# Optimization experiments

Hardware: AMD Instinct MI355X
Metric: run time of the kernel (lower is better)

The kernel has to match this reference:

```python
import jax, jax.numpy as jnp
import numpy as np

K = 1024          # num_embeddings
D = 64            # embedding_dim
TEMP = 1.0        # cfg.temperature
EPS = 1e-10


def setup_inputs() -> dict:
    key = jax.random.key(0)
    k1, k2 = jax.random.split(key)
    return {
        "inputs": jax.random.normal(k1, (16, 2048, D), dtype=jnp.float32),
        "embedding": jax.random.normal(k2, (K, D), dtype=jnp.float32),
        "code_count": jnp.ones((K,), dtype=jnp.float32),
    }


def _distances(flat, embedding):
    return ((flat ** 2).sum(axis=1, keepdims=True)
            + (embedding ** 2).sum(axis=1)
            - 2.0 * flat @ embedding.T)


def reference(inputs, embedding, code_count):
    B = inputs.shape[0]
    flat = inputs.reshape(-1, D)                      # [N, D]
    N = flat.shape[0]

    d = _distances(flat, embedding)                   # [N, K]
    idx = jnp.argmin(d, axis=1)                       # [N]

    # one-hot @ codebook == gather by index
    quantized = embedding[idx].reshape(inputs.shape)

    commitment_loss = jnp.mean((jax.lax.stop_gradient(quantized) - inputs) ** 2)

    # ortho loss over used codes (code_count >= 1), via masking (jit-safe)
    mask = (code_count >= 1.0).astype(inputs.dtype)   # [K]
    n_used = mask.sum()
    normed = embedding / jnp.clip(
        jnp.linalg.norm(embedding, axis=1, keepdims=True), 1e-12)
    normed = normed * mask[:, None]                   # zero out unused rows
    cos = normed @ normed.T                           # [K, K]
    ortho_loss = (cos ** 2).sum() / (n_used ** 2) - 1.0 / n_used

    # entropy loss over softmax(-d / T)
    prob = jax.nn.softmax(-d / TEMP, axis=1)          # [N, K]
    entropy_loss = -jnp.mean(jnp.sum(prob * jnp.log(prob + EPS), axis=1))
    entropy_loss = entropy_loss / jnp.log2(jnp.asarray(K, inputs.dtype))

    # straight-through estimator
    quantized_st = inputs + jax.lax.stop_gradient(quantized - inputs)

    # perplexity from code usage histogram (mean of one-hot encodings)
    avg_probs = jnp.zeros((K,), inputs.dtype).at[idx].add(1.0) / N
    perplexity = jnp.exp(-jnp.sum(avg_probs * jnp.log(avg_probs + EPS)))

    coverage = mask.sum() / K
    indices = idx.reshape(B, -1)

    return (quantized_st, commitment_loss, ortho_loss, entropy_loss,
            perplexity, coverage, indices)
```

## Files before the change

### kernel.cpp

```cpp
#include <hip/hip_runtime.h>
#include <math.h>

#define N_ROWS  32768
#define K_CODES 1024
#define D_DIM   64
#define NSPLIT  4
#define C_SHIFT 30.0f
#define LOG2E_F 1.4426950408889634f
#define LN2_F   0.6931471805599453f
#define TAU     0.25f

#define WS_CNT    0
#define WS_E2C    6144
#define PART_STRIDE (NSPLIT * N_ROWS)
#define WS_PART_S  8192
#define WS_PART_U  (8192 + PART_STRIDE)
#define WS_PART_M1 (8192 + 2 * PART_STRIDE)
#define WS_PART_M2 (8192 + 3 * PART_STRIDE)
#define CHUNK_F4  260
#define MAIN_CHUNKS 16
#define WS_EB      (8192 + 4 * PART_STRIDE)
#define WS_GP      (WS_EB + 64 * CHUNK_F4 * 4)
#define WS_HB      (WS_GP + 16 * 4096)
#define WS_PH      (WS_HB + 16 * K_CODES)
#define WS_PC      (WS_PH + 512)

#define OUT_Q      0
#define OUT_COMMIT 2097152
#define OUT_ORTHO  2097153
#define OUT_ENT    2097154
#define OUT_PERP   2097155
#define OUT_COV    2097156
#define OUT_IDX    2097157

typedef __attribute__((ext_vector_type(8))) _Float16 f16x8;
typedef __attribute__((ext_vector_type(4))) float f32x4;

__device__ inline unsigned umaxu(unsigned a, unsigned b) { return a > b ? a : b; }
__device__ inline unsigned uminu(unsigned a, unsigned b) { return a < b ? a : b; }

__device__ inline float keyval(unsigned u) {
    unsigned b = (u & 0x80000000u) ? (u ^ 0x80000000u) : ~u;
    return __uint_as_float(b);
}

__device__ inline void decomp2x8(const float* v, f16x8& h, f16x8& m) {
#pragma unroll
    for (int i = 0; i < 8; ++i) {
        _Float16 hh = (_Float16)v[i];
        h[i] = hh;
        m[i] = (_Float16)(v[i] - (float)hh);
    }
}

__global__ __launch_bounds__(256) void vq_prep_ortho(const float* __restrict__ emb,
                                                     const float* __restrict__ cc,
                                                     float* __restrict__ ws) {
    __shared__ float srows[64][64];
    __shared__ float rn2[64];
    const int t = threadIdx.x;

    if (blockIdx.x < 16) {
        if (blockIdx.x == 0 && t == 0) ((int*)ws)[WS_CNT] = 0;

        const int tid  = blockIdx.x * 256 + t;
        const int c    = tid >> 6;
        const int lane = tid & 63;
        const int col  = lane & 15;
        const int kg   = lane >> 4;
        const int code = c * 16 + col;
        float4* EB4 = (float4*)(ws + WS_EB);
#pragma unroll
        for (int s = 0; s < 2; ++s) {
            const float* ep = emb + (size_t)code * D_DIM + s * 32 + kg * 8;
            float4 A4 = *(const float4*)ep;
            float4 B4 = *(const float4*)(ep + 4);
            float v[8] = {A4.x, A4.y, A4.z, A4.w, B4.x, B4.y, B4.z, B4.w};
            union { f16x8 h; float4 f; } th, tm;
            decomp2x8(v, th.h, tm.h);
            const int base = c * CHUNK_F4;
            EB4[base + (s * 2 + 0) * 64 + lane] = th.f;
            EB4[base + (s * 2 + 1) * 64 + lane] = tm.f;
        }
        if (kg == 0) {
            const float4* e4 = (const float4*)(emb + (size_t)code * D_DIM);
            float ssum = 0.f;
#pragma unroll
            for (int j = 0; j < 16; ++j) {
                float4 v = e4[j];
                ssum += v.x * v.x + v.y * v.y + v.z * v.z + v.w * v.w;
            }
            float e2c = ssum + C_SHIFT;
            ws[WS_E2C + code] = e2c;
            ((float*)(EB4 + c * CHUNK_F4 + 256))[col] = e2c * LOG2E_F;
        }
        return;
    }

    const int ob = blockIdx.x - 16;
    const int k0 = ob * 64;
    const int rb = t >> 4;
    const int c4 = (t & 15) << 2;

#pragma unroll
    for (int i = 0; i < 4; ++i) {
        const int r = i * 16 + rb;
        float4 v = *(const float4*)(emb + (size_t)(k0 + r) * D_DIM + c4);
        *(float4*)(&srows[r][c4]) = v;
        float ss = v.x * v.x + v.y * v.y + v.z * v.z + v.w * v.w;
        ss += __shfl_down(ss, 8, 16);
        ss += __shfl_down(ss, 4, 16);
        ss += __shfl_down(ss, 2, 16);
        ss += __shfl_down(ss, 1, 16);
        if ((t & 15) == 0) {
            float nrm = fmaxf(sqrtf(ss), 1e-12f);
            float m = (cc[k0 + r] >= 1.0f) ? 1.0f : 0.0f;
            rn2[r] = m / (nrm * nrm);
        }
    }
    __syncthreads();

    const int a  = t >> 2;
    const int b0 = (t & 3) << 4;
    float acc[16];
#pragma unroll
    for (int i = 0; i < 16; ++i) acc[i] = 0.f;

#pragma unroll 4
    for (int k = 0; k < 64; ++k) {
        float na = srows[k][a] * rn2[k];
        const float* rbp = &srows[k][b0];
#pragma unroll
        for (int i = 0; i < 16; ++i) acc[i] = fmaf(na, rbp[i], acc[i]);
    }
#pragma unroll
    for (int i = 0; i < 16; ++i)
        ws[WS_GP + ob * 4096 + a * 64 + b0 + i] = acc[i];
}

#define MFMA_F16 __builtin_amdgcn_mfma_f32_16x16x32_f16

__global__ __launch_bounds__(256)
void vq_main(const float* __restrict__ inp, float* __restrict__ ws) {
    __shared__ float4 sbuf[3][256];
    const int t    = threadIdx.x;
    const int lane = t & 63;
    const int wave = t >> 6;
    const int col  = lane & 15;
    const int kg   = lane >> 4;
    const int rg   = blockIdx.x >> 2;
    const int sp   = blockIdx.x & 3;
    const int row  = rg * 64 + wave * 16 + col;

    f16x8 xh0, xm0, xh1, xm1;
    {
        const float* xp = inp + (size_t)row * D_DIM + kg * 8;
        float4 A4 = *(const float4*)xp;
        float4 B4 = *(const float4*)(xp + 4);
        float v[8] = {A4.x, A4.y, A4.z, A4.w, B4.x, B4.y, B4.z, B4.w};
        decomp2x8(v, xh0, xm0);
        A4 = *(const float4*)(xp + 32);
        B4 = *(const float4*)(xp + 36);
        float w[8] = {A4.x, A4.y, A4.z, A4.w, B4.x, B4.y, B4.z, B4.w};
        decomp2x8(w, xh1, xm1);
    }

    const float4* EBp = (const float4*)(ws + WS_EB)
                      + (size_t)sp * MAIN_CHUNKS * CHUNK_F4;

    float sa[4], ua[4];
    unsigned m1[4], m2[4];
#pragma unroll
    for (int q = 0; q < 4; ++q) {
        sa[q] = 0.f; ua[q] = 0.f;
        m1[q] = 0u; m2[q] = 0u;
    }

    sbuf[0][t] = EBp[t];
    sbuf[1][t] = EBp[CHUNK_F4 + t];

#pragma unroll 1
    for (int c = 0; c < MAIN_CHUNKS; ++c) {
        __syncthreads();
        float4 gn;
        if (c + 2 < MAIN_CHUNKS) gn = EBp[(size_t)(c + 2) * CHUNK_F4 + t];

        const f16x8* pb = (const f16x8*)&sbuf[c % 3][0];
        const float e2v = ((const float*)(EBp + (size_t)c * CHUNK_F4 + 256))[col];

        f32x4 acc = {0.f, 0.f, 0.f, 0.f};
        {
            f16x8 bh0 = pb[0 * 64 + lane];
            f16x8 bm0 = pb[1 * 64 + lane];
            acc = MFMA_F16(xh0, bh0, acc, 0, 0, 0);
            acc = MFMA_F16(xm0, bh0, acc, 0, 0, 0);
            acc = MFMA_F16(xh0, bm0, acc, 0, 0, 0);
            acc = MFMA_F16(xm0, bm0, acc, 0, 0, 0);
        }
        {
            f16x8 bh1 = pb[2 * 64 + lane];
            f16x8 bm1 = pb[3 * 64 + lane];
            acc = MFMA_F16(xh1, bh1, acc, 0, 0, 0);
            acc = MFMA_F16(xm1, bh1, acc, 0, 0, 0);
            acc = MFMA_F16(xh1, bm1, acc, 0, 0, 0);
            acc = MFMA_F16(xm1, bm1, acc, 0, 0, 0);
        }

        const unsigned embedv = 255u - (unsigned)(c * 16 + col);
#pragma unroll
        for (int q = 0; q < 4; ++q) {
            float g = fmaf(2.0f * LOG2E_F, acc[q], -e2v);
            float pw;
            asm("v_exp_f32 %0, %1" : "=v"(pw) : "v"(g));
            sa[q] += pw;
            ua[q] = fmaf(pw, g, ua[q]);
            int gb = __float_as_int(g);
            unsigned u = (unsigned)(gb ^ ((gb >> 31) | 0x80000000));
            unsigned key = (u & 0xFFFFFF00u) | embedv;
            m2[q] = uminu(umaxu(key, m2[q]), m1[q]);
            m1[q] = umaxu(m1[q], key);
        }

        if (c + 2 < MAIN_CHUNKS) sbuf[(c + 2) % 3][t] = gn;
    }

#pragma unroll
    for (int off = 1; off < 16; off <<= 1) {
#pragma unroll
        for (int q = 0; q < 4; ++q) {
            sa[q] += __shfl_xor(sa[q], off);
            ua[q] += __shfl_xor(ua[q], off);
            unsigned p1 = (unsigned)__shfl_xor((int)m1[q], off);
            unsigned p2 = (unsigned)__shfl_xor((int)m2[q], off);
            unsigned lo = uminu(m1[q], p1);
            m1[q] = umaxu(m1[q], p1);
            m2[q] = umaxu(lo, umaxu(m2[q], p2));
        }
    }

    if (col == 0) {
#pragma unroll
        for (int q = 0; q < 4; ++q) {
            const int r  = rg * 64 + wave * 16 + kg * 4 + q;
            const int pi = sp * N_ROWS + r;
            ws[WS_PART_S  + pi] = sa[q];
            ws[WS_PART_U  + pi] = ua[q];
            ws[WS_PART_M1 + pi] = __uint_as_float(m1[q]);
            ws[WS_PART_M2 + pi] = __uint_as_float(m2[q]);
        }
    }
}

__global__ __launch_bounds__(256) void vq_combine(const float* __restrict__ inp,
                                                  const float* __restrict__ emb,
                                                  float* __restrict__ ws,
                                                  float* __restrict__ out) {
    __shared__ float shH[4], shC[4];
    const int t    = threadIdx.x;
    const int lane = t & 63;
    const int wave = t >> 6;
    const int l    = t & 3;
    const int row  = blockIdx.x * 64 + (t >> 2);
    const int qb   = lane & ~3;

    const int pi = l * N_ROWS + row;
    float    Sl = ws[WS_PART_S  + pi];
    float    Ul = ws[WS_PART_U  + pi];
    unsigned K1 = __float_as_uint(ws[WS_PART_M1 + pi]);
    unsigned K2 = __float_as_uint(ws[WS_PART_M2 + pi]);
    float    G1 = keyval(K1);

    float S = 0.f, U2 = 0.f, Gmax = -1e30f;
#pragma unroll
    for (int k = 0; k < 4; ++k) {
        S  += __shfl(Sl, qb + k);
        U2 += __shfl(Ul, qb + k);
        Gmax = fmaxf(Gmax, __shfl(G1, qb + k));
    }

    float4 Xq[4];
    const float4* xr = (const float4*)(inp + (size_t)row * D_DIM);
#pragma unroll
    for (int k = 0; k < 4; ++k) Xq[k] = xr[l + 4 * k];

    float bestg = -1e30f; int I = K_CODES;
#pragma unroll 1
    for (int j = 0; j < 8; ++j) {
        const int sp = j >> 1;
        const unsigned kk = (unsigned)__shfl((int)((j & 1) ? K2 : K1), qb + sp);
        const float v = keyval(kk);
        if (v < Gmax - TAU) continue;
        const int c = sp * 256 + 255 - (int)(kk & 255u);
        const float4* e4 = (const float4*)(emb + (size_t)c * D_DIM);
        float d = 0.f;
#pragma unroll
        for (int k = 0; k < 4; ++k) {
            float4 ev = e4[l + 4 * k];
            float4 xv = Xq[k];
            d = fmaf(ev.x, xv.x, d); d = fmaf(ev.y, xv.y, d);
            d = fmaf(ev.z, xv.z, d); d = fmaf(ev.w, xv.w, d);
        }
        float dA = __shfl(d, qb + 0) + __shfl(d, qb + 1);
        float dB = __shfl(d, qb + 2) + __shfl(d, qb + 3);
        float g  = fmaf(2.0f, dA + dB, -ws[WS_E2C + c]);
        if (g > bestg || (g == bestg && c < I)) { bestg = g; I = c; }
    }

    float H = logf(S) - (U2 * LN2_F) / S;

    if (l == 0) out[OUT_IDX + row] = (float)I;

    const float4* q4 = (const float4*)(emb + (size_t)I * D_DIM);
    float4* oq = (float4*)out + (size_t)row * 16;
    float cs = 0.f;
#pragma unroll
    for (int k = 0; k < 4; ++k) {
        float4 q = q4[l + 4 * k], x = Xq[k];
        float dx = q.x - x.x, dy = q.y - x.y, dz = q.z - x.z, dw = q.w - x.w;
        cs += dx * dx + dy * dy + dz * dz + dw * dw;
        float4 o;
        o.x = x.x + dx; o.y = x.y + dy; o.z = x.z + dz; o.w = x.w + dw;
        oq[l + 4 * k] = o;
    }

    float Hc = (l == 0) ? H : 0.f;
#pragma unroll
    for (int off = 32; off; off >>= 1) {
        Hc += __shfl_down(Hc, off);
        cs += __shfl_down(cs, off);
    }
    if (lane == 0) { shH[wave] = Hc; shC[wave] = cs; }
    __syncthreads();
    if (t == 0) {
        ws[WS_PH + blockIdx.x] = shH[0] + shH[1] + shH[2] + shH[3];
        ws[WS_PC + blockIdx.x] = shC[0] + shC[1] + shC[2] + shC[3];
    }
}

__global__ __launch_bounds__(256) void vq_hist_fin(const float* __restrict__ cc,
                                                   float* __restrict__ ws,
                                                   float* __restrict__ out) {
    __shared__ int h[K_CODES];
    __shared__ int lastFlag;
    __shared__ float red[5][4];
    const int t = threadIdx.x;
#pragma unroll
    for (int i = 0; i < 4; ++i) h[t + 256 * i] = 0;
    __syncthreads();
    const int base = blockIdx.x * 2048;
#pragma unroll
    for (int i = 0; i < 8; ++i) {
        int idx = (int)out[OUT_IDX + base + t + 256 * i];
        atomicAdd(&h[idx], 1);
    }
    __syncthreads();
#pragma unroll
    for (int i = 0; i < 4; ++i) {
        const int k = t + 256 * i;
        ws[WS_HB + blockIdx.x * K_CODES + k] = (float)h[k];
    }
    __threadfence();
    __syncthreads();
    if (t == 0) {
        int old = __hip_atomic_fetch_add((int*)ws + WS_CNT, 1,
                                         __ATOMIC_ACQ_REL,
                                         __HIP_MEMORY_SCOPE_AGENT);
        lastFlag = (old == 15);
    }
    __syncthreads();
    if (!lastFlag) return;

    float hp = 0.f, gg = 0.f, nu = 0.f, hh = 0.f, cm = 0.f;
    for (int k = t; k < K_CODES; k += 256) {
        float s = 0.f;
#pragma unroll
        for (int b = 0; b < 16; ++b)
            s += __hip_atomic_load(ws + WS_HB + b * K_CODES + k,
                                   __ATOMIC_RELAXED, __HIP_MEMORY_SCOPE_AGENT);
        float p = s * (1.0f / (float)N_ROWS);
        hp += p * logf(p + 1e-10f);
        nu += (cc[k] >= 1.0f) ? 1.0f : 0.0f;
    }
    for (int i = t; i < 4096; i += 256) {
        float s = 0.f;
#pragma unroll
        for (int b = 0; b < 16; ++b) s += ws[WS_GP + b * 4096 + i];
        gg = fmaf(s, s, gg);
    }
    for (int i = t; i < 512; i += 256) {
        hh += ws[WS_PH + i];
        cm += ws[WS_PC + i];
    }
#pragma unroll
    for (int off = 32; off; off >>= 1) {
        hp += __shfl_down(hp, off);
        gg += __shfl_down(gg, off);
        nu += __shfl_down(nu, off);
        hh += __shfl_down(hh, off);
        cm += __shfl_down(cm, off);
    }
    if ((t & 63) == 0) {
        const int w = t >> 6;
        red[0][w] = hp; red[1][w] = gg; red[2][w] = nu;
        red[3][w] = hh; red[4][w] = cm;
    }
    __syncthreads();
    if (t == 0) {
        float hsum = red[0][0] + red[0][1] + red[0][2] + red[0][3];
        float gsum = red[1][0] + red[1][1] + red[1][2] + red[1][3];
        float nuv  = red[2][0] + red[2][1] + red[2][2] + red[2][3];
        float hacc = red[3][0] + red[3][1] + red[3][2] + red[3][3];
        float cacc = red[4][0] + red[4][1] + red[4][2] + red[4][3];
        out[OUT_PERP]   = expf(-hsum);
        out[OUT_ENT]    = hacc * (1.0f / (float)N_ROWS) * 0.1f;
        out[OUT_COMMIT] = cacc * (1.0f / ((float)N_ROWS * (float)D_DIM));
        out[OUT_ORTHO]  = gsum / (nuv * nuv) - 1.0f / nuv;
        out[OUT_COV]    = nuv * (1.0f / (float)K_CODES);
    }
}

extern "C" void kernel_launch(void* const* d_in, const int* in_sizes, int n_in,
                              void* d_out, int out_size, void* d_ws, size_t ws_size,
                              hipStream_t stream) {
    const float* inp = (const float*)d_in[0];
    const float* emb = (const float*)d_in[1];
    const float* cc  = (const float*)d_in[2];
    float* out = (float*)d_out;
    float* ws  = (float*)d_ws;

    vq_prep_ortho<<<32, 256, 0, stream>>>(emb, cc, ws);
    vq_main<<<(N_ROWS / 64) * NSPLIT, 256, 0, stream>>>(inp, ws);
    vq_combine<<<N_ROWS / 64, 256, 0, stream>>>(inp, emb, ws, out);
    vq_hist_fin<<<16, 256, 0, stream>>>(cc, ws, out);
}
```

Before: 119.8 us.

## Fuse combine stage into main kernel and drop codebook split across blocks

Each block now scans all 1024 codes itself instead of splitting the codebook four ways across blocks, keeping per-quarter top-2 keys and the softmax partial sums in shared memory. The argmin rescoring, quantized output and loss partials that used to live in a separate combine kernel now run in the tail of the main kernel. This removes one launch and the global round trip of partial results. In exchange, the grid shrinks from 2048 to 512 blocks, which reduces parallelism and latency hiding, and each block runs a longer serial chunk loop.

```diff
diff --git a/kernel.cpp b/kernel.cpp
--- a/kernel.cpp
+++ b/kernel.cpp
@@ -4,7 +4,6 @@
 #define N_ROWS  32768
 #define K_CODES 1024
 #define D_DIM   64
-#define NSPLIT  4
 #define C_SHIFT 30.0f
 #define LOG2E_F 1.4426950408889634f
 #define LN2_F   0.6931471805599453f
@@ -12,14 +11,9 @@
 
 #define WS_CNT    0
 #define WS_E2C    6144
-#define PART_STRIDE (NSPLIT * N_ROWS)
-#define WS_PART_S  8192
-#define WS_PART_U  (8192 + PART_STRIDE)
-#define WS_PART_M1 (8192 + 2 * PART_STRIDE)
-#define WS_PART_M2 (8192 + 3 * PART_STRIDE)
 #define CHUNK_F4  260
-#define MAIN_CHUNKS 16
-#define WS_EB      (8192 + 4 * PART_STRIDE)
+#define ALL_CHUNKS 64
+#define WS_EB      8192
 #define WS_GP      (WS_EB + 64 * CHUNK_F4 * 4)
 #define WS_HB      (WS_GP + 16 * 4096)
 #define WS_PH      (WS_HB + 16 * K_CODES)
@@ -141,15 +135,18 @@
 #define MFMA_F16 __builtin_amdgcn_mfma_f32_16x16x32_f16
 
 __global__ __launch_bounds__(256)
-void vq_main(const float* __restrict__ inp, float* __restrict__ ws) {
+void vq_main(const float* __restrict__ inp, const float* __restrict__ emb,
+             float* __restrict__ ws, float* __restrict__ out) {
     __shared__ float4 sbuf[3][256];
+    __shared__ unsigned cK[4][16][4][2];
+    __shared__ float sS[4][16], sU[4][16];
+    __shared__ float shH[4], shC[4];
     const int t    = threadIdx.x;
     const int lane = t & 63;
     const int wave = t >> 6;
     const int col  = lane & 15;
     const int kg   = lane >> 4;
-    const int rg   = blockIdx.x >> 2;
-    const int sp   = blockIdx.x & 3;
+    const int rg   = blockIdx.x;
     const int row  = rg * 64 + wave * 16 + col;
 
     f16x8 xh0, xm0, xh1, xm1;
@@ -165,8 +162,7 @@
         decomp2x8(w, xh1, xm1);
     }
 
-    const float4* EBp = (const float4*)(ws + WS_EB)
-                      + (size_t)sp * MAIN_CHUNKS * CHUNK_F4;
+    const float4* EBp = (const float4*)(ws + WS_EB);
 
     float sa[4], ua[4];
     unsigned m1[4], m2[4];
@@ -180,10 +176,10 @@
     sbuf[1][t] = EBp[CHUNK_F4 + t];
 
 #pragma unroll 1
-    for (int c = 0; c < MAIN_CHUNKS; ++c) {
+    for (int c = 0; c < ALL_CHUNKS; ++c) {
         __syncthreads();
         float4 gn;
-        if (c + 2 < MAIN_CHUNKS) gn = EBp[(size_t)(c + 2) * CHUNK_F4 + t];
+        if (c + 2 < ALL_CHUNKS) gn = EBp[(size_t)(c + 2) * CHUNK_F4 + t];
 
         const f16x8* pb = (const f16x8*)&sbuf[c % 3][0];
         const float e2v = ((const float*)(EBp + (size_t)c * CHUNK_F4 + 256))[col];
@@ -206,7 +202,7 @@
             acc = MFMA_F16(xm1, bm1, acc, 0, 0, 0);
         }
 
-        const unsigned embedv = 255u - (unsigned)(c * 16 + col);
+        const unsigned embedv = 255u - (unsigned)((c & 15) * 16 + col);
 #pragma unroll
         for (int q = 0; q < 4; ++q) {
             float g = fmaf(2.0f * LOG2E_F, acc[q], -e2v);
@@ -221,7 +217,31 @@
             m1[q] = umaxu(m1[q], key);
         }
 
-        if (c + 2 < MAIN_CHUNKS) sbuf[(c + 2) % 3][t] = gn;
+        if ((c & 15) == 15) {
+            const int qt = c >> 4;
+#pragma unroll
+            for (int off = 1; off < 16; off <<= 1) {
+#pragma unroll
+                for (int q = 0; q < 4; ++q) {
+                    unsigned p1 = (unsigned)__shfl_xor((int)m1[q], off);
+                    unsigned p2 = (unsigned)__shfl_xor((int)m2[q], off);
+                    unsigned lo = uminu(m1[q], p1);
+                    m1[q] = umaxu(m1[q], p1);
+                    m2[q] = umaxu(lo, umaxu(m2[q], p2));
+                }
+            }
+            if (col == 0) {
+#pragma unroll
+                for (int q = 0; q < 4; ++q) {
+                    cK[wave][kg * 4 + q][qt][0] = m1[q];
+                    cK[wave][kg * 4 + q][qt][1] = m2[q];
+                }
+            }
+#pragma unroll
+            for (int q = 0; q < 4; ++q) { m1[q] = 0u; m2[q] = 0u; }
+        }
+
+        if (c + 2 < ALL_CHUNKS) sbuf[(c + 2) % 3][t] = gn;
     }
 
 #pragma unroll
@@ -230,67 +250,43 @@
         for (int q = 0; q < 4; ++q) {
             sa[q] += __shfl_xor(sa[q], off);
             ua[q] += __shfl_xor(ua[q], off);
-            unsigned p1 = (unsigned)__shfl_xor((int)m1[q], off);
-            unsigned p2 = (unsigned)__shfl_xor((int)m2[q], off);
-            unsigned lo = uminu(m1[q], p1);
-            m1[q] = umaxu(m1[q], p1);
-            m2[q] = umaxu(lo, umaxu(m2[q], p2));
-        }
-    }
-
+        }
+    }
     if (col == 0) {
 #pragma unroll
         for (int q = 0; q < 4; ++q) {
-            const int r  = rg * 64 + wave * 16 + kg * 4 + q;
-            const int pi = sp * N_ROWS + r;
-            ws[WS_PART_S  + pi] = sa[q];
-            ws[WS_PART_U  + pi] = ua[q];
-            ws[WS_PART_M1 + pi] = __uint_as_float(m1[q]);
-            ws[WS_PART_M2 + pi] = __uint_as_float(m2[q]);
-        }
-    }
-}
-
-__global__ __launch_bounds__(256) void vq_combine(const float* __restrict__ inp,
-                                                  const float* __restrict__ emb,
-                                                  float* __restrict__ ws,
-                                                  float* __restrict__ out) {
-    __shared__ float shH[4], shC[4];
-    const int t    = threadIdx.x;
-    const int lane = t & 63;
-    const int wave = t >> 6;
+            sS[wave][kg * 4 + q] = sa[q];
+            sU[wave][kg * 4 + q] = ua[q];
+        }
+    }
+    __syncthreads();
+
     const int l    = t & 3;
-    const int row  = blockIdx.x * 64 + (t >> 2);
+    const int rloc = (t >> 2) & 15;
+    const int wsrc = t >> 6;
+    const int frow = rg * 64 + wsrc * 16 + rloc;
     const int qb   = lane & ~3;
 
-    const int pi = l * N_ROWS + row;
-    float    Sl = ws[WS_PART_S  + pi];
-    float    Ul = ws[WS_PART_U  + pi];
-    unsigned K1 = __float_as_uint(ws[WS_PART_M1 + pi]);
-    unsigned K2 = __float_as_uint(ws[WS_PART_M2 + pi]);
-    float    G1 = keyval(K1);
-
-    float S = 0.f, U2 = 0.f, Gmax = -1e30f;
-#pragma unroll
-    for (int k = 0; k < 4; ++k) {
-        S  += __shfl(Sl, qb + k);
-        U2 += __shfl(Ul, qb + k);
-        Gmax = fmaxf(Gmax, __shfl(G1, qb + k));
-    }
+    float S  = sS[wsrc][rloc];
+    float U2 = sU[wsrc][rloc];
+
+    float Gmax = -1e30f;
+#pragma unroll
+    for (int qt = 0; qt < 4; ++qt)
+        Gmax = fmaxf(Gmax, keyval(cK[wsrc][rloc][qt][0]));
 
     float4 Xq[4];
-    const float4* xr = (const float4*)(inp + (size_t)row * D_DIM);
+    const float4* xr = (const float4*)(inp + (size_t)frow * D_DIM);
 #pragma unroll
     for (int k = 0; k < 4; ++k) Xq[k] = xr[l + 4 * k];
 
     float bestg = -1e30f; int I = K_CODES;
 #pragma unroll 1
     for (int j = 0; j < 8; ++j) {
-        const int sp = j >> 1;
-        const unsigned kk = (unsigned)__shfl((int)((j & 1) ? K2 : K1), qb + sp);
+        const unsigned kk = cK[wsrc][rloc][j >> 1][j & 1];
         const float v = keyval(kk);
         if (v < Gmax - TAU) continue;
-        const int c = sp * 256 + 255 - (int)(kk & 255u);
+        const int c = (j >> 1) * 256 + 255 - (int)(kk & 255u);
         const float4* e4 = (const float4*)(emb + (size_t)c * D_DIM);
         float d = 0.f;
 #pragma unroll
@@ -308,10 +304,10 @@
 
     float H = logf(S) - (U2 * LN2_F) / S;
 
-    if (l == 0) out[OUT_IDX + row] = (float)I;
+    if (l == 0) out[OUT_IDX + frow] = (float)I;
 
     const float4* q4 = (const float4*)(emb + (size_t)I * D_DIM);
-    float4* oq = (float4*)out + (size_t)row * 16;
+    float4* oq = (float4*)out + (size_t)frow * 16;
     float cs = 0.f;
 #pragma unroll
     for (int k = 0; k < 4; ++k) {
@@ -429,7 +425,6 @@
     float* ws  = (float*)d_ws;
 
     vq_prep_ortho<<<32, 256, 0, stream>>>(emb, cc, ws);
-    vq_main<<<(N_ROWS / 64) * NSPLIT, 256, 0, stream>>>(inp, ws);
-    vq_combine<<<N_ROWS / 64, 256, 0, stream>>>(inp, emb, ws, out);
+    vq_main<<<N_ROWS / 64, 256, 0, stream>>>(inp, emb, ws, out);
     vq_hist_fin<<<16, 256, 0, stream>>>(cc, ws, out);
 }
```

Result: slower. 124.0 us (+3.5%).
